# Kernel tuning notes

Measured on AMD Instinct MI355X. Metric: run time of the kernel, lower is better.

Reference implementation:

```python
import jax, jax.numpy as jnp
import numpy as np

N, E, F_IN, H, D, C = 50000, 800000, 128, 4, 64, 40
HD = H * D
NEG_SLOPE = 0.2


def setup_inputs() -> dict:
    key = jax.random.key(0)
    ks = jax.random.split(key, 16)
    x = jax.random.normal(ks[0], (N, F_IN), dtype=jnp.float32)
    edge_index = jax.random.randint(ks[1], (2, E), 0, N, dtype=jnp.int64)
    def glorot(k, shape):
        fan = shape[0] + shape[-1]
        return jax.random.normal(k, shape, dtype=jnp.float32) * jnp.sqrt(2.0 / fan)
    params = {
        'W1': glorot(ks[2], (F_IN, HD)), 'as1': glorot(ks[3], (H, D)), 'ad1': glorot(ks[4], (H, D)), 'b1': jnp.zeros((HD,), jnp.float32),
        'W2': glorot(ks[5], (HD, HD)),   'as2': glorot(ks[6], (H, D)), 'ad2': glorot(ks[7], (H, D)), 'b2': jnp.zeros((HD,), jnp.float32),
        'W3': glorot(ks[8], (HD, HD)),   'as3': glorot(ks[9], (H, D)), 'ad3': glorot(ks[10], (H, D)), 'b3': jnp.zeros((HD,), jnp.float32),
        'Wl': glorot(ks[11], (HD, C)),   'bl': jnp.zeros((C,), jnp.float32),
    }
    return {'x': x, 'edge_index': edge_index, **params}


def gat_layer(x, src, dst, W, a_src, a_dst, b):
    # x: [N, F] -> h: [N, H, D]
    h = (x @ W).reshape(N, H, D)
    alpha_s = jnp.sum(h * a_src, axis=-1)  # [N, H]
    alpha_d = jnp.sum(h * a_dst, axis=-1)  # [N, H]
    e = alpha_s[src] + alpha_d[dst]        # [E', H]
    e = jnp.where(e > 0, e, NEG_SLOPE * e)  # leaky_relu
    # segment softmax over destination nodes
    m = jax.ops.segment_max(e, dst, num_segments=N)  # [N, H]
    m = jnp.where(jnp.isfinite(m), m, 0.0)
    ex = jnp.exp(e - m[dst])
    s = jax.ops.segment_sum(ex, dst, num_segments=N)  # [N, H]
    att = ex / (s[dst] + 1e-16)                        # [E', H]
    # weighted scatter-aggregate of source features
    out = jax.ops.segment_sum(h[src] * att[:, :, None], dst, num_segments=N)  # [N, H, D]
    return out.reshape(N, HD) + b


def reference(x, edge_index, W1, as1, ad1, b1, W2, as2, ad2, b2, W3, as3, ad3, b3, Wl, bl):
    # PyG GATConv adds self-loops by default
    loops = jnp.arange(N, dtype=edge_index.dtype)
    src = jnp.concatenate([edge_index[0], loops])
    dst = jnp.concatenate([edge_index[1], loops])
    # dropout is identity in eval mode
    h = jax.nn.elu(gat_layer(x, src, dst, W1, as1, ad1, b1))
    h = jax.nn.elu(gat_layer(h, src, dst, W2, as2, ad2, b2))
    h = jax.nn.elu(gat_layer(h, src, dst, W3, as3, ad3, b3))
    logits = h @ Wl + bl
    return jax.nn.log_softmax(logits, axis=1)
```

## Files before the change

kernel.cpp:

```cpp
#include <hip/hip_runtime.h>
#include <math.h>

#define NN 50000
#define NE 800000
#define ET (NE + NN)
#define FIN 128
#define HDIM 256
#define NHEAD 4
#define NCLS 40
#define NEG 0.2f
#define NB_SCAN ((NN + 255) / 256)
#define NB_CONV 3125
#define NB_WCONV 192
#define NB_EDGE ((ET + 255) / 256)

typedef short bf16x8 __attribute__((ext_vector_type(8)));
typedef float f32x4 __attribute__((ext_vector_type(4)));

__device__ __forceinline__ unsigned short f2b(float f) {
    unsigned int u = __float_as_uint(f);
    unsigned int r = (u + 0x7fffu + ((u >> 16) & 1u)) >> 16;
    return (unsigned short)r;
}
__device__ __forceinline__ unsigned int cvtpk(float lo, float hi) {
    unsigned int r;
    asm volatile("v_cvt_pk_bf16_f32 %0, %1, %2" : "=v"(r) : "v"(lo), "v"(hi));
    return r;
}
__device__ __forceinline__ float b2f(unsigned short u) {
    unsigned int x = ((unsigned int)u) << 16;
    return __uint_as_float(x);
}

__device__ __forceinline__ int sniff_is64(const int* __restrict__ ei32, int* s64p) {
    if (threadIdx.x < 64) {
        int nz = ei32[1 + 2 * threadIdx.x] | ei32[129 + 2 * threadIdx.x];
        unsigned long long b = __ballot(nz != 0);
        if (threadIdx.x == 0) *s64p = (b == 0ull) ? 1 : 0;
    }
    __syncthreads();
    return *s64p;
}

__device__ __forceinline__ int load_node(const int* ei32, int is64, long long idx) {
    return is64 ? ei32[2 * idx] : ei32[idx];
}

__global__ __launch_bounds__(256) void prep_kernel(const float* __restrict__ x,
                                                   unsigned short* __restrict__ xb,
                                                   const float* __restrict__ W1,
                                                   const float* __restrict__ W2,
                                                   const float* __restrict__ W3,
                                                   unsigned short* __restrict__ Wt1,
                                                   unsigned short* __restrict__ Wt2,
                                                   unsigned short* __restrict__ Wt3,
                                                   const int* __restrict__ ei32,
                                                   int* __restrict__ deg) {
    __shared__ float sm[32][33];
    __shared__ int s64;
    int bid = blockIdx.x;
    if (bid < NB_CONV) {
        int i = (bid * 256 + threadIdx.x) * 8;
        if (i + 8 > NN * FIN) return;
        float4 f0 = *(const float4*)(x + i);
        float4 f1 = *(const float4*)(x + i + 4);
        uint4 pk;
        pk.x = cvtpk(f0.x, f0.y);
        pk.y = cvtpk(f0.z, f0.w);
        pk.z = cvtpk(f1.x, f1.y);
        pk.w = cvtpk(f1.z, f1.w);
        *(uint4*)(xb + i) = pk;
    } else if (bid < NB_CONV + NB_WCONV) {
        int wb = bid - NB_CONV;
        int z = wb >> 6;
        int ky = (wb >> 3) & 7;
        int nx = wb & 7;
        const float* W = (z == 0) ? W1 : (z == 1) ? W2 : W3;
        unsigned short* Wt = (z == 0) ? Wt1 : (z == 1) ? Wt2 : Wt3;
        int K = (z == 0) ? FIN : HDIM;
        int k0 = ky * 32;
        if (k0 >= K) return;
        int tx = threadIdx.x & 31, ty = threadIdx.x >> 5;
        int n0 = nx * 32;
#pragma unroll
        for (int j = 0; j < 4; j++)
            sm[ty + j * 8][tx] = W[(size_t)(k0 + ty + j * 8) * HDIM + n0 + tx];
        __syncthreads();
#pragma unroll
        for (int j = 0; j < 4; j++)
            Wt[(size_t)(n0 + ty + j * 8) * K + k0 + tx] = f2b(sm[tx][ty + j * 8]);
    } else {
        int is64 = sniff_is64(ei32, &s64);
        int e = (bid - NB_CONV - NB_WCONV) * 256 + threadIdx.x;
        if (e >= ET) return;
        int d = (e < NE) ? load_node(ei32, is64, (long long)NE + e) : (e - NE);
        atomicAdd(&deg[d], 1);
    }
}

__global__ void scan1(const int* __restrict__ deg, int* __restrict__ incl,
                      int* __restrict__ bsum) {
    __shared__ int sm[256];
    int i = blockIdx.x * 256 + threadIdx.x;
    int v = (i < NN) ? deg[i] : 0;
    sm[threadIdx.x] = v;
    __syncthreads();
    for (int o = 1; o < 256; o <<= 1) {
        int add = (threadIdx.x >= o) ? sm[threadIdx.x - o] : 0;
        __syncthreads();
        sm[threadIdx.x] += add;
        __syncthreads();
    }
    if (i < NN) incl[i] = sm[threadIdx.x];
    if (threadIdx.x == 255) bsum[blockIdx.x] = sm[255];
}

__global__ void scan2(int* __restrict__ bsum) {
    __shared__ int sm[256];
    int t = threadIdx.x;
    sm[t] = (t < NB_SCAN) ? bsum[t] : 0;
    __syncthreads();
    if (t == 0) {
        int run = 0;
        for (int b = 0; b < NB_SCAN; b++) { int v = sm[b]; sm[b] = run; run += v; }
    }
    __syncthreads();
    if (t < NB_SCAN) bsum[t] = sm[t];
}

__global__ void scan3(const int* __restrict__ incl, const int* __restrict__ bsum,
                      const int* __restrict__ deg, int* __restrict__ indptr,
                      int* __restrict__ cursor) {
    int i = blockIdx.x * 256 + threadIdx.x;
    if (i < NN) {
        int v = bsum[blockIdx.x] + incl[i];
        indptr[i + 1] = v;
        cursor[i] = v - deg[i];
    }
    if (i == 0) indptr[0] = 0;
}

__global__ void fill_kernel(const int* __restrict__ ei32,
                            int* __restrict__ cursor, int* __restrict__ esrc) {
    __shared__ int s64;
    int is64 = sniff_is64(ei32, &s64);
    int e = blockIdx.x * blockDim.x + threadIdx.x;
    if (e >= ET) return;
    int s, d;
    if (e < NE) {
        s = load_node(ei32, is64, (long long)e);
        d = load_node(ei32, is64, (long long)NE + e);
    } else {
        s = d = e - NE;
    }
    int pos = atomicAdd(&cursor[d], 1);
    esrc[pos] = s;
}

__global__ __launch_bounds__(256) void gemm_mfma(const unsigned short* __restrict__ A,
                                                 const unsigned short* __restrict__ Bt,
                                                 unsigned short* __restrict__ Cb,
                                                 const float* __restrict__ a_s,
                                                 const float* __restrict__ a_d,
                                                 float* __restrict__ als,
                                                 float* __restrict__ ald,
                                                 int M, int K) {
    __shared__ unsigned short As[128][72];
    __shared__ unsigned short Bs[64][72];
    int bid = blockIdx.x;
    int xcd = bid & 7, g = bid >> 3;
    int cblk = g & 3, rg = g >> 2;
    int rblk = rg * 8 + xcd;
    int r0 = rblk * 128, n0 = cblk * 64;
    if (r0 >= M) return;

    int t = threadIdx.x;
    int lane = t & 63, wid = t >> 6;

    f32x4 acc[2][4];
#pragma unroll
    for (int m = 0; m < 2; m++)
#pragma unroll
        for (int n = 0; n < 4; n++)
            acc[m][n] = (f32x4){0.f, 0.f, 0.f, 0.f};

    int ar = t >> 1, ah = (t & 1) * 32;
    int arow = r0 + ar; if (arow > M - 1) arow = M - 1;
    const unsigned short* ga = A + (size_t)arow * K + ah;
    int bn = t >> 2, bq = (t & 3) * 16;
    const unsigned short* gb = Bt + (size_t)(n0 + bn) * K + bq;

    int fr = lane & 15;
    int kf = (lane >> 4) * 8;

    for (int k0 = 0; k0 < K; k0 += 64) {
#pragma unroll
        for (int j = 0; j < 4; j++)
            *(uint4*)&As[ar][ah + j * 8] = *(const uint4*)(ga + k0 + j * 8);
#pragma unroll
        for (int j = 0; j < 2; j++)
            *(uint4*)&Bs[bn][bq + j * 8] = *(const uint4*)(gb + k0 + j * 8);
        __syncthreads();
#pragma unroll
        for (int kk = 0; kk < 64; kk += 32) {
            bf16x8 a[2], b[4];
#pragma unroll
            for (int m = 0; m < 2; m++)
                a[m] = *(const bf16x8*)&As[wid * 32 + m * 16 + fr][kk + kf];
#pragma unroll
            for (int n = 0; n < 4; n++)
                b[n] = *(const bf16x8*)&Bs[n * 16 + fr][kk + kf];
#pragma unroll
            for (int m = 0; m < 2; m++)
#pragma unroll
                for (int n = 0; n < 4; n++)
                    acc[m][n] = __builtin_amdgcn_mfma_f32_16x16x32_bf16(a[m], b[n], acc[m][n], 0, 0, 0);
        }
        __syncthreads();
    }

    int rbase = r0 + wid * 32 + (lane >> 4) * 4;
    int cbase = n0 + fr;
    int head = n0 >> 6;
    float asv[4], adv[4];
#pragma unroll
    for (int n = 0; n < 4; n++) {
        asv[n] = a_s[cbase + n * 16];
        adv[n] = a_d[cbase + n * 16];
    }
#pragma unroll
    for (int m = 0; m < 2; m++)
#pragma unroll
        for (int q = 0; q < 4; q++) {
            int gr = rbase + m * 16 + q;
            float vs = 0.f, vd = 0.f;
#pragma unroll
            for (int n = 0; n < 4; n++) {
                float v = acc[m][n][q];
                vs += v * asv[n];
                vd += v * adv[n];
            }
#pragma unroll
            for (int o = 8; o > 0; o >>= 1) {
                vs += __shfl_xor(vs, o);
                vd += __shfl_xor(vd, o);
            }
            if (fr == 0 && gr < M) {
                als[gr * NHEAD + head] = vs;
                ald[gr * NHEAD + head] = vd;
            }
        }

    unsigned short (*Cs)[68] = (unsigned short(*)[68])&As[0][0];
    int lr0 = wid * 32 + (lane >> 4) * 4;
#pragma unroll
    for (int m = 0; m < 2; m++)
#pragma unroll
        for (int q = 0; q < 4; q++)
#pragma unroll
            for (int n = 0; n < 4; n++)
                Cs[lr0 + m * 16 + q][fr + n * 16] = f2b(acc[m][n][q]);
    __syncthreads();
    int tr = t >> 4;
    int tc = (t & 15) * 4;
#pragma unroll
    for (int rr = 0; rr < 8; rr++) {
        int lr = tr + rr * 16;
        int gr = r0 + lr;
        if (gr < M) *(ushort4*)(Cb + (size_t)gr * HDIM + n0 + tc) = *(const ushort4*)&Cs[lr][tc];
    }
}

__global__ __launch_bounds__(256) void agg_kernel(const unsigned short* __restrict__ projb,
                                                  const float* __restrict__ als,
                                                  const float* __restrict__ ald,
                                                  const int* __restrict__ indptr,
                                                  const int* __restrict__ esrc,
                                                  const float* __restrict__ bias,
                                                  unsigned short* __restrict__ featb) {
    int wid = threadIdx.x >> 6;
    int v = blockIdx.x * 4 + wid;
    if (v >= NN) return;
    int lane = threadIdx.x & 63;
    int h = lane >> 4;
    int sub = lane & 15;
    int beg = indptr[v], end = indptr[v + 1];
    float adv = ald[v * NHEAD + h];

    float e0 = 0.f, e1 = 0.f;
    int s0r = 0, s1r = 0;
    float m = -INFINITY, ss = 0.f;
    int idx = 0;
    for (int i = beg + sub; i < end; i += 16, idx++) {
        int s = esrc[i];
        float e = als[s * NHEAD + h] + adv;
        e = e > 0.f ? e : NEG * e;
        if (idx == 0) { e0 = e; s0r = s; }
        else if (idx == 1) { e1 = e; s1r = s; }
        if (e > m) {
            ss = ss * __expf(m - e) + 1.f;
            m = e;
        } else {
            ss += __expf(e - m);
        }
    }
#pragma unroll
    for (int o = 8; o > 0; o >>= 1) {
        float m2 = __shfl_xor(m, o);
        float s2 = __shfl_xor(ss, o);
        float mn = fmaxf(m, m2);
        float a = (m == mn) ? ss : ss * __expf(m - mn);
        float b = (m2 == mn) ? s2 : s2 * __expf(m2 - mn);
        m = mn;
        ss = a + b;
    }
    float inv = 1.f / (ss + 1e-16f);

    float4 acc = make_float4(0.f, 0.f, 0.f, 0.f);
    int c = beg;
    int chunk = 0;
    for (; c + 16 < end; c += 32, chunk += 2) {
        int remB = end - (c + 16); if (remB > 16) remB = 16;
        int sA, sB;
        float eA, eB;
        if (chunk == 0) {
            sA = s0r; eA = e0;
            sB = s1r; eB = e1;
        } else {
            sA = esrc[c + sub];
            eA = als[sA * NHEAD + h] + adv;
            eA = eA > 0.f ? eA : NEG * eA;
            int iB = c + 16 + (sub < remB ? sub : remB - 1);
            sB = esrc[iB];
            eB = als[sB * NHEAD + h] + adv;
            eB = eB > 0.f ? eB : NEG * eB;
        }
        float wA = __expf(eA - m) * inv;
        float wB = (sub < remB) ? __expf(eB - m) * inv : 0.f;

        ushort4 pA[16], pB[16];
#pragma unroll
        for (int j = 0; j < 16; j++) {
            int s = __shfl(sA, j);
            pA[j] = *(const ushort4*)(projb + (size_t)s * HDIM + (lane << 2));
        }
#pragma unroll
        for (int j = 0; j < 16; j++) {
            int s = __shfl(sB, j);
            pB[j] = *(const ushort4*)(projb + (size_t)s * HDIM + (lane << 2));
        }
#pragma unroll
        for (int j = 0; j < 16; j++) {
            float w = __shfl(wA, (h << 4) | j);
            acc.x += b2f(pA[j].x) * w;
            acc.y += b2f(pA[j].y) * w;
            acc.z += b2f(pA[j].z) * w;
            acc.w += b2f(pA[j].w) * w;
        }
#pragma unroll
        for (int j = 0; j < 16; j++) {
            float w = __shfl(wB, (h << 4) | j);
            acc.x += b2f(pB[j].x) * w;
            acc.y += b2f(pB[j].y) * w;
            acc.z += b2f(pB[j].z) * w;
            acc.w += b2f(pB[j].w) * w;
        }
    }
    if (c < end) {
        int rem = end - c;
        int sA;
        float eA;
        if (chunk == 0) { sA = s0r; eA = e0; }
        else if (chunk == 1) { sA = s1r; eA = e1; }
        else {
            int i = c + (sub < rem ? sub : rem - 1);
            sA = esrc[i];
            eA = als[sA * NHEAD + h] + adv;
            eA = eA > 0.f ? eA : NEG * eA;
        }
        float wA = (sub < rem) ? __expf(eA - m) * inv : 0.f;
        ushort4 p[16];
#pragma unroll
        for (int j = 0; j < 16; j++) {
            int s = __shfl(sA, j);
            p[j] = *(const ushort4*)(projb + (size_t)s * HDIM + (lane << 2));
        }
#pragma unroll
        for (int j = 0; j < 16; j++) {
            float w = __shfl(wA, (h << 4) | j);
            acc.x += b2f(p[j].x) * w;
            acc.y += b2f(p[j].y) * w;
            acc.z += b2f(p[j].z) * w;
            acc.w += b2f(p[j].w) * w;
        }
    }

    const float4 b4 = *(const float4*)(bias + (lane << 2));
    float4 r;
    r.x = acc.x + b4.x;
    r.y = acc.y + b4.y;
    r.z = acc.z + b4.z;
    r.w = acc.w + b4.w;
    r.x = r.x > 0.f ? r.x : __expf(r.x) - 1.f;
    r.y = r.y > 0.f ? r.y : __expf(r.y) - 1.f;
    r.z = r.z > 0.f ? r.z : __expf(r.z) - 1.f;
    r.w = r.w > 0.f ? r.w : __expf(r.w) - 1.f;
    uint2 o2;
    o2.x = cvtpk(r.x, r.y);
    o2.y = cvtpk(r.z, r.w);
    *(uint2*)(featb + (size_t)v * HDIM + (lane << 2)) = o2;
}

__global__ __launch_bounds__(256) void final_kernel(const unsigned short* __restrict__ featb,
                                                    const float* __restrict__ Wl,
                                                    const float* __restrict__ bl,
                                                    float* __restrict__ out) {
    const int BK = 16;
    __shared__ float As[BK][65];
    __shared__ float Bs[BK][65];
    int tx = threadIdx.x & 15, ty = threadIdx.x >> 4;
    int row0 = blockIdx.x * 64;
    float acc[4][4] = {};
    for (int k0 = 0; k0 < HDIM; k0 += BK) {
#pragma unroll
        for (int i = 0; i < 4; i++) {
            int l = threadIdx.x + 256 * i;
            int r = l >> 4, c = l & 15;
            int gr = row0 + r;
            float v = 0.f;
            if (gr < NN) v = b2f(featb[(size_t)gr * HDIM + k0 + c]);
            As[c][r] = v;
        }
#pragma unroll
        for (int i = 0; i < 4; i++) {
            int l = threadIdx.x + 256 * i;
            int r = l >> 6, c = l & 63;
            Bs[r][c] = (c < NCLS) ? Wl[(size_t)(k0 + r) * NCLS + c] : 0.f;
        }
        __syncthreads();
#pragma unroll
        for (int k = 0; k < BK; k++) {
            float a[4], b[4];
#pragma unroll
            for (int i = 0; i < 4; i++) a[i] = As[k][ty + 16 * i];
#pragma unroll
            for (int j = 0; j < 4; j++) b[j] = Bs[k][tx + 16 * j];
#pragma unroll
            for (int i = 0; i < 4; i++)
#pragma unroll
                for (int j = 0; j < 4; j++) acc[i][j] += a[i] * b[j];
        }
        __syncthreads();
    }
    float b0 = bl[tx], b1 = bl[tx + 16], b2 = (tx < 8) ? bl[tx + 32] : 0.f;
#pragma unroll
    for (int i = 0; i < 4; i++) {
        int gr = row0 + ty + 16 * i;
        if (gr >= NN) continue;
        float l0 = acc[i][0] + b0;
        float l1 = acc[i][1] + b1;
        float l2 = (tx < 8) ? acc[i][2] + b2 : -INFINITY;
        float m = fmaxf(fmaxf(l0, l1), l2);
#pragma unroll
        for (int o = 8; o > 0; o >>= 1) m = fmaxf(m, __shfl_xor(m, o));
        float s = __expf(l0 - m) + __expf(l1 - m) + ((tx < 8) ? __expf(l2 - m) : 0.f);
#pragma unroll
        for (int o = 8; o > 0; o >>= 1) s += __shfl_xor(s, o);
        float lse = m + __logf(s);
        out[(size_t)gr * NCLS + tx] = l0 - lse;
        out[(size_t)gr * NCLS + tx + 16] = l1 - lse;
        if (tx < 8) out[(size_t)gr * NCLS + tx + 32] = l2 - lse;
    }
}

extern "C" void kernel_launch(void* const* d_in, const int* in_sizes, int n_in,
                              void* d_out, int out_size, void* d_ws, size_t ws_size,
                              hipStream_t stream) {
    const float* x  = (const float*)d_in[0];
    const int* ei32 = (const int*)d_in[1];
    const float* W1 = (const float*)d_in[2];
    const float* as1 = (const float*)d_in[3];
    const float* ad1 = (const float*)d_in[4];
    const float* b1 = (const float*)d_in[5];
    const float* W2 = (const float*)d_in[6];
    const float* as2 = (const float*)d_in[7];
    const float* ad2 = (const float*)d_in[8];
    const float* b2 = (const float*)d_in[9];
    const float* W3 = (const float*)d_in[10];
    const float* as3 = (const float*)d_in[11];
    const float* ad3 = (const float*)d_in[12];
    const float* b3 = (const float*)d_in[13];
    const float* Wl = (const float*)d_in[14];
    const float* bl = (const float*)d_in[15];
    float* out = (float*)d_out;

    char* w = (char*)d_ws;
    unsigned short* projb = (unsigned short*)w;  w += (size_t)NN * HDIM * 2;
    unsigned short* featb = (unsigned short*)w;  w += (size_t)NN * HDIM * 2;
    unsigned short* xb    = (unsigned short*)w;  w += (size_t)NN * FIN * 2;
    unsigned short* Wt1b  = (unsigned short*)w;  w += (size_t)HDIM * FIN * 2;
    unsigned short* Wt2b  = (unsigned short*)w;  w += (size_t)HDIM * HDIM * 2;
    unsigned short* Wt3b  = (unsigned short*)w;  w += (size_t)HDIM * HDIM * 2;
    float* als  = (float*)w;  w += (size_t)NN * NHEAD * 4;
    float* ald  = (float*)w;  w += (size_t)NN * NHEAD * 4;
    int* deg    = (int*)w;    w += (size_t)NN * 4;
    int* incl   = (int*)w;    w += (size_t)NN * 4;
    int* bsum   = (int*)w;    w += 256 * 4;
    int* indptr = (int*)w;    w += (size_t)(NN + 1) * 4;
    int* cursor = (int*)w;    w += (size_t)NN * 4;
    int* esrc   = (int*)w;    w += (size_t)ET * 4;

    hipMemsetAsync(deg, 0, (size_t)NN * 4, stream);
    prep_kernel<<<NB_CONV + NB_WCONV + NB_EDGE, 256, 0, stream>>>(
        x, xb, W1, W2, W3, Wt1b, Wt2b, Wt3b, ei32, deg);

    scan1<<<NB_SCAN, 256, 0, stream>>>(deg, incl, bsum);
    scan2<<<1, 256, 0, stream>>>(bsum);
    scan3<<<NB_SCAN, 256, 0, stream>>>(incl, bsum, deg, indptr, cursor);
    fill_kernel<<<NB_EDGE, 256, 0, stream>>>(ei32, cursor, esrc);

    int ggrid = 8 * 4 * (((NN + 127) / 128 + 7) / 8);
    int agrid = (NN + 3) / 4;

    gemm_mfma<<<ggrid, 256, 0, stream>>>(xb, Wt1b, projb, as1, ad1, als, ald, NN, FIN);
    agg_kernel<<<agrid, 256, 0, stream>>>(projb, als, ald, indptr, esrc, b1, featb);
    gemm_mfma<<<ggrid, 256, 0, stream>>>(featb, Wt2b, projb, as2, ad2, als, ald, NN, HDIM);
    agg_kernel<<<agrid, 256, 0, stream>>>(projb, als, ald, indptr, esrc, b2, featb);
    gemm_mfma<<<ggrid, 256, 0, stream>>>(featb, Wt3b, projb, as3, ad3, als, ald, NN, HDIM);
    agg_kernel<<<agrid, 256, 0, stream>>>(projb, als, ald, indptr, esrc, b3, featb);
    final_kernel<<<(NN + 63) / 64, 256, 0, stream>>>(featb, Wl, bl, out);
}
```

Baseline: 404.1 us.

## Widen GEMM tiles to 128x128 with 512 threads and fuse edge fill into layer-1 GEMM

Each GEMM block now uses 8 waves to compute a 128x128 output tile instead of 128x64 with 4 waves, so every A tile is loaded half as often and each block covers two heads. The CSR fill pass is merged into the first GEMM launch as extra blocks, which removes one kernel launch and lets the atomic scatter overlap with the GEMM. The cost is larger shared memory per block and 512-thread blocks, which may lower occupancy. The merged launch also mixes GEMM and scatter blocks with different resource needs.

Result: slower. 430.2 us (+6.5%).

```diff
diff --git a/kernel.cpp b/kernel.cpp
--- a/kernel.cpp
+++ b/kernel.cpp
@@ -13,6 +13,8 @@
 #define NB_CONV 3125
 #define NB_WCONV 192
 #define NB_EDGE ((ET + 255) / 256)
+#define NB_FILL ((ET + 511) / 512)
+#define GG ( 8 * 2 * (((NN + 127) / 128 + 7) / 8) )
 
 typedef short bf16x8 __attribute__((ext_vector_type(8)));
 typedef float f32x4 __attribute__((ext_vector_type(4)));
@@ -140,42 +142,26 @@
     if (i == 0) indptr[0] = 0;
 }
 
-__global__ void fill_kernel(const int* __restrict__ ei32,
-                            int* __restrict__ cursor, int* __restrict__ esrc) {
-    __shared__ int s64;
-    int is64 = sniff_is64(ei32, &s64);
-    int e = blockIdx.x * blockDim.x + threadIdx.x;
-    if (e >= ET) return;
-    int s, d;
-    if (e < NE) {
-        s = load_node(ei32, is64, (long long)e);
-        d = load_node(ei32, is64, (long long)NE + e);
-    } else {
-        s = d = e - NE;
-    }
-    int pos = atomicAdd(&cursor[d], 1);
-    esrc[pos] = s;
-}
-
-__global__ __launch_bounds__(256) void gemm_mfma(const unsigned short* __restrict__ A,
-                                                 const unsigned short* __restrict__ Bt,
-                                                 unsigned short* __restrict__ Cb,
-                                                 const float* __restrict__ a_s,
-                                                 const float* __restrict__ a_d,
-                                                 float* __restrict__ als,
-                                                 float* __restrict__ ald,
-                                                 int M, int K) {
+__device__ __forceinline__ void gemm_body(const unsigned short* __restrict__ A,
+                                          const unsigned short* __restrict__ Bt,
+                                          unsigned short* __restrict__ Cb,
+                                          const float* __restrict__ a_s,
+                                          const float* __restrict__ a_d,
+                                          float* __restrict__ als,
+                                          float* __restrict__ ald,
+                                          int M, int K, int bid) {
     __shared__ unsigned short As[128][72];
-    __shared__ unsigned short Bs[64][72];
-    int bid = blockIdx.x;
+    __shared__ unsigned short Bs[128][72];
     int xcd = bid & 7, g = bid >> 3;
-    int cblk = g & 3, rg = g >> 2;
+    int cblk = g & 1, rg = g >> 1;
     int rblk = rg * 8 + xcd;
-    int r0 = rblk * 128, n0 = cblk * 64;
+    int r0 = rblk * 128, n0 = cblk * 128;
     if (r0 >= M) return;
 
     int t = threadIdx.x;
-    int lane = t & 63, wid = t >> 6;
+    int lane = t & 63, w8 = t >> 6;
+    int wr = w8 & 3, wc = w8 >> 2;
+    int fr = lane & 15, kg = lane >> 4, kf = kg * 8;
 
     f32x4 acc[2][4];
 #pragma unroll
@@ -184,32 +170,29 @@
         for (int n = 0; n < 4; n++)
             acc[m][n] = (f32x4){0.f, 0.f, 0.f, 0.f};
 
-    int ar = t >> 1, ah = (t & 1) * 32;
-    int arow = r0 + ar; if (arow > M - 1) arow = M - 1;
-    const unsigned short* ga = A + (size_t)arow * K + ah;
-    int bn = t >> 2, bq = (t & 3) * 16;
-    const unsigned short* gb = Bt + (size_t)(n0 + bn) * K + bq;
-
-    int fr = lane & 15;
-    int kf = (lane >> 4) * 8;
+    int s0 = t, s1 = t + 512;
+    int ar0 = r0 + (s0 >> 3); if (ar0 > M - 1) ar0 = M - 1;
+    int ar1 = r0 + (s1 >> 3); if (ar1 > M - 1) ar1 = M - 1;
+    const unsigned short* gA0 = A + (size_t)ar0 * K + (s0 & 7) * 8;
+    const unsigned short* gA1 = A + (size_t)ar1 * K + (s1 & 7) * 8;
+    const unsigned short* gB0 = Bt + (size_t)(n0 + (s0 >> 3)) * K + (s0 & 7) * 8;
+    const unsigned short* gB1 = Bt + (size_t)(n0 + (s1 >> 3)) * K + (s1 & 7) * 8;
 
     for (int k0 = 0; k0 < K; k0 += 64) {
-#pragma unroll
-        for (int j = 0; j < 4; j++)
-            *(uint4*)&As[ar][ah + j * 8] = *(const uint4*)(ga + k0 + j * 8);
-#pragma unroll
-        for (int j = 0; j < 2; j++)
-            *(uint4*)&Bs[bn][bq + j * 8] = *(const uint4*)(gb + k0 + j * 8);
+        *(uint4*)&As[s0 >> 3][(s0 & 7) * 8] = *(const uint4*)(gA0 + k0);
+        *(uint4*)&As[s1 >> 3][(s1 & 7) * 8] = *(const uint4*)(gA1 + k0);
+        *(uint4*)&Bs[s0 >> 3][(s0 & 7) * 8] = *(const uint4*)(gB0 + k0);
+        *(uint4*)&Bs[s1 >> 3][(s1 & 7) * 8] = *(const uint4*)(gB1 + k0);
         __syncthreads();
 #pragma unroll
         for (int kk = 0; kk < 64; kk += 32) {
             bf16x8 a[2], b[4];
 #pragma unroll
             for (int m = 0; m < 2; m++)
-                a[m] = *(const bf16x8*)&As[wid * 32 + m * 16 + fr][kk + kf];
+                a[m] = *(const bf16x8*)&As[wr * 32 + m * 16 + fr][kk + kf];
 #pragma unroll
             for (int n = 0; n < 4; n++)
-                b[n] = *(const bf16x8*)&Bs[n * 16 + fr][kk + kf];
+                b[n] = *(const bf16x8*)&Bs[wc * 64 + n * 16 + fr][kk + kf];
 #pragma unroll
             for (int m = 0; m < 2; m++)
 #pragma unroll
@@ -219,20 +202,18 @@
         __syncthreads();
     }
 
-    int rbase = r0 + wid * 32 + (lane >> 4) * 4;
-    int cbase = n0 + fr;
-    int head = n0 >> 6;
+    int head = cblk * 2 + wc;
     float asv[4], adv[4];
 #pragma unroll
     for (int n = 0; n < 4; n++) {
-        asv[n] = a_s[cbase + n * 16];
-        adv[n] = a_d[cbase + n * 16];
+        asv[n] = a_s[n0 + wc * 64 + n * 16 + fr];
+        adv[n] = a_d[n0 + wc * 64 + n * 16 + fr];
     }
 #pragma unroll
     for (int m = 0; m < 2; m++)
 #pragma unroll
         for (int q = 0; q < 4; q++) {
-            int gr = rbase + m * 16 + q;
+            int gr = r0 + wr * 32 + m * 16 + kg * 4 + q;
             float vs = 0.f, vd = 0.f;
 #pragma unroll
             for (int n = 0; n < 4; n++) {
@@ -251,23 +232,64 @@
             }
         }
 
-    unsigned short (*Cs)[68] = (unsigned short(*)[68])&As[0][0];
-    int lr0 = wid * 32 + (lane >> 4) * 4;
+    unsigned short (*Cs)[136] = (unsigned short(*)[136])&As[0][0];
 #pragma unroll
     for (int m = 0; m < 2; m++)
 #pragma unroll
         for (int q = 0; q < 4; q++)
 #pragma unroll
             for (int n = 0; n < 4; n++)
-                Cs[lr0 + m * 16 + q][fr + n * 16] = f2b(acc[m][n][q]);
+                Cs[wr * 32 + m * 16 + kg * 4 + q][wc * 64 + n * 16 + fr] = f2b(acc[m][n][q]);
     __syncthreads();
-    int tr = t >> 4;
-    int tc = (t & 15) * 4;
-#pragma unroll
-    for (int rr = 0; rr < 8; rr++) {
-        int lr = tr + rr * 16;
-        int gr = r0 + lr;
-        if (gr < M) *(ushort4*)(Cb + (size_t)gr * HDIM + n0 + tc) = *(const ushort4*)&Cs[lr][tc];
+    int row = t >> 2, u = t & 3;
+    int gr = r0 + row;
+    if (gr < M) {
+#pragma unroll
+        for (int j = 0; j < 4; j++) {
+            int col0 = u * 32 + j * 8;
+            *(uint4*)(Cb + (size_t)gr * HDIM + n0 + col0) = *(const uint4*)&Cs[row][col0];
+        }
+    }
+}
+
+__global__ __launch_bounds__(512) void gemm_mfma(const unsigned short* __restrict__ A,
+                                                 const unsigned short* __restrict__ Bt,
+                                                 unsigned short* __restrict__ Cb,
+                                                 const float* __restrict__ a_s,
+                                                 const float* __restrict__ a_d,
+                                                 float* __restrict__ als,
+                                                 float* __restrict__ ald,
+                                                 int M, int K) {
+    gemm_body(A, Bt, Cb, a_s, a_d, als, ald, M, K, blockIdx.x);
+}
+
+__global__ __launch_bounds__(512) void gemm1_fill_kernel(const unsigned short* __restrict__ A,
+                                                         const unsigned short* __restrict__ Bt,
+                                                         unsigned short* __restrict__ Cb,
+                                                         const float* __restrict__ a_s,
+                                                         const float* __restrict__ a_d,
+                                                         float* __restrict__ als,
+                                                         float* __restrict__ ald,
+                                                         const int* __restrict__ ei32,
+                                                         int* __restrict__ cursor,
+                                                         int* __restrict__ esrc) {
+    __shared__ int s64;
+    int bid = blockIdx.x;
+    if (bid < GG) {
+        gemm_body(A, Bt, Cb, a_s, a_d, als, ald, NN, FIN, bid);
+    } else {
+        int is64 = sniff_is64(ei32, &s64);
+        int e = (bid - GG) * 512 + threadIdx.x;
+        if (e >= ET) return;
+        int s, d;
+        if (e < NE) {
+            s = load_node(ei32, is64, (long long)e);
+            d = load_node(ei32, is64, (long long)NE + e);
+        } else {
+            s = d = e - NE;
+        }
+        int pos = atomicAdd(&cursor[d], 1);
+        esrc[pos] = s;
     }
 }
 
@@ -517,16 +539,15 @@
     scan1<<<NB_SCAN, 256, 0, stream>>>(deg, incl, bsum);
     scan2<<<1, 256, 0, stream>>>(bsum);
     scan3<<<NB_SCAN, 256, 0, stream>>>(incl, bsum, deg, indptr, cursor);
-    fill_kernel<<<NB_EDGE, 256, 0, stream>>>(ei32, cursor, esrc);
-
-    int ggrid = 8 * 4 * (((NN + 127) / 128 + 7) / 8);
+
     int agrid = (NN + 3) / 4;
 
-    gemm_mfma<<<ggrid, 256, 0, stream>>>(xb, Wt1b, projb, as1, ad1, als, ald, NN, FIN);
+    gemm1_fill_kernel<<<GG + NB_FILL, 512, 0, stream>>>(
+        xb, Wt1b, projb, as1, ad1, als, ald, ei32, cursor, esrc);
     agg_kernel<<<agrid, 256, 0, stream>>>(projb, als, ald, indptr, esrc, b1, featb);
-    gemm_mfma<<<ggrid, 256, 0, stream>>>(featb, Wt2b, projb, as2, ad2, als, ald, NN, HDIM);
+    gemm_mfma<<<GG, 512, 0, stream>>>(featb, Wt2b, projb, as2, ad2, als, ald, NN, HDIM);
     agg_kernel<<<agrid, 256, 0, stream>>>(projb, als, ald, indptr, esrc, b2, featb);
-    gemm_mfma<<<ggrid, 256, 0, stream>>>(featb, Wt3b, projb, as3, ad3, als, ald, NN, HDIM);
+    gemm_mfma<<<GG, 512, 0, stream>>>(featb, Wt3b, projb, as3, ad3, als, ald, NN, HDIM);
     agg_kernel<<<agrid, 256, 0, stream>>>(projb, als, ald, indptr, esrc, b3, featb);
     final_kernel<<<(NN + 63) / 64, 256, 0, stream>>>(featb, Wl, bl, out);
 }
```
